# Kernel tuning notes

Measured on AMD Instinct MI355X. Metric: run time of the kernel, lower is better.

Reference implementation:

```python
import jax, jax.numpy as jnp
import numpy as np

N = 50000
E = 600000
D = 128
EPS = 1e-5  # nn.LayerNorm default eps


def gcn_conv(x, W, b, src, dst):
    # PyG GCNConv with add_self_loops=True, edge_weight=None (all ones),
    # symmetric normalization D^-1/2 (A+I) D^-1/2.
    h = x @ W                                        # [N, D]
    deg = jnp.zeros((N,), h.dtype).at[dst].add(1.0) + 1.0  # +1 for self loop
    dinv = jax.lax.rsqrt(deg)                        # deg >= 1, safe
    norm = dinv[src] * dinv[dst]                     # [E]
    msg = h[src] * norm[:, None]                     # [E, D] gather
    agg = jax.ops.segment_sum(msg, dst, num_segments=N)
    agg = agg + h * (dinv * dinv)[:, None]           # self-loop term
    return agg + b


def layer_norm(x, g, b):
    mu = jnp.mean(x, axis=-1, keepdims=True)
    var = jnp.mean(jnp.square(x - mu), axis=-1, keepdims=True)
    return (x - mu) * jax.lax.rsqrt(var + EPS) * g + b


def setup_inputs() -> dict:
    key = jax.random.key(0)
    ks = jax.random.split(key, 6)
    x = jax.random.normal(ks[0], (N, D), dtype=jnp.float32)
    edge_index = jax.random.randint(ks[1], (2, E), 0, N, dtype=jnp.int64)
    s = 1.0 / np.sqrt(D)
    W1 = jax.random.uniform(ks[2], (D, D), jnp.float32, -s, s)
    W2 = jax.random.uniform(ks[3], (D, D), jnp.float32, -s, s)
    b1 = jnp.zeros((D,), jnp.float32)
    b2 = jnp.zeros((D,), jnp.float32)
    ln1_g = jnp.ones((D,), jnp.float32)
    ln1_b = jnp.zeros((D,), jnp.float32)
    ln2_g = jnp.ones((D,), jnp.float32)
    ln2_b = jnp.zeros((D,), jnp.float32)
    return {"x": x, "edge_index": edge_index, "W1": W1, "b1": b1,
            "ln1_g": ln1_g, "ln1_b": ln1_b, "W2": W2, "b2": b2,
            "ln2_g": ln2_g, "ln2_b": ln2_b}


def reference(x, edge_index, W1, b1, ln1_g, ln1_b, W2, b2, ln2_g, ln2_b):
    src, dst = edge_index[0], edge_index[1]
    out = gcn_conv(x, W1, b1, src, dst)
    out = jax.nn.relu(layer_norm(out, ln1_g, ln1_b))  # dropout = identity (eval)
    out = gcn_conv(out, W2, b2, src, dst)
    out = jax.nn.relu(layer_norm(out, ln2_g, ln2_b))
    return out + x
```

## Files before the change

### kernel.cpp

```cpp
#include <hip/hip_runtime.h>
#include <hip/hip_fp16.h>

#define D 128
#define EPS 1e-5f
#define KB 64
#define NBSH 7
#define BUCKW 128

typedef unsigned int u32;
typedef unsigned short u16;
typedef unsigned char u8;
typedef __attribute__((ext_vector_type(8))) _Float16 half8;
typedef __attribute__((ext_vector_type(4))) float f32x4;
typedef __attribute__((ext_vector_type(2))) float f32x2;

__device__ inline u16 f2h(float x) {
  _Float16 t = (_Float16)x;
  return __builtin_bit_cast(u16, t);
}
__device__ inline u8 f2fp8(float x) {
  return (u8)(__builtin_amdgcn_cvt_pk_fp8_f32(x, x, 0, false) & 0xff);
}

__global__ __launch_bounds__(256) void k_prep(const float* __restrict__ W1,
                                              const float* __restrict__ W2,
                                              u16* __restrict__ Wt1,
                                              u16* __restrict__ Wt2) {
  int i = blockIdx.x * 256 + threadIdx.x;
  if (i < 2 * D * D) {
    const float* W = (i < D * D) ? W1 : W2;
    u16* Wt = (i < D * D) ? Wt1 : Wt2;
    int ii = i & (D * D - 1);
    int k = ii >> 7, c = ii & 127;
    Wt[c * D + k] = f2h(W[ii]);
  }
}

template <bool F32IN>
__device__ __forceinline__ void gemm_body(const void* __restrict__ in_,
                                          const u16* __restrict__ Wt,
                                          u8* __restrict__ out, int nrows,
                                          int blk) {
  const int tid = threadIdx.x;
  const int lane = tid & 63, wv = tid >> 6;
  const int m = lane & 15, q = lane >> 4;
  const int r0 = blk * 64 + wv * 16;
  const int rowa = min(r0 + m, nrows - 1);

  f32x4 acc[8];
#pragma unroll
  for (int ct = 0; ct < 8; ct++) acc[ct] = (f32x4)(0.0f);

#pragma unroll
  for (int kk = 0; kk < 4; kk++) {
    const int kbase = kk * 32 + q * 8;
    half8 a;
    if (F32IN) {
      const float* in = (const float*)in_;
      float4 v0 = *(const float4*)(in + (size_t)rowa * D + kbase);
      float4 v1 = *(const float4*)(in + (size_t)rowa * D + kbase + 4);
      a[0] = (_Float16)v0.x; a[1] = (_Float16)v0.y;
      a[2] = (_Float16)v0.z; a[3] = (_Float16)v0.w;
      a[4] = (_Float16)v1.x; a[5] = (_Float16)v1.y;
      a[6] = (_Float16)v1.z; a[7] = (_Float16)v1.w;
    } else {
      const u16* in = (const u16*)in_;
      a = *(const half8*)(in + (size_t)rowa * D + kbase);
    }
#pragma unroll
    for (int ct = 0; ct < 8; ct++) {
      half8 b = *(const half8*)(Wt + (ct * 16 + m) * D + kbase);
      acc[ct] = __builtin_amdgcn_mfma_f32_16x16x32_f16(a, b, acc[ct], 0, 0, 0);
    }
  }

#pragma unroll
  for (int ct = 0; ct < 8; ct++) {
#pragma unroll
    for (int rg = 0; rg < 4; rg++) {
      int rr = r0 + q * 4 + rg;
      if (rr < nrows) out[(size_t)rr * D + ct * 16 + m] = f2fp8(acc[ct][rg]);
    }
  }
}

__global__ __launch_bounds__(256) void k_count_gemm1(
    const int* __restrict__ dst, int* __restrict__ cnt, int E, int NB, int EPB,
    const float* __restrict__ x, const u16* __restrict__ Wt1,
    u8* __restrict__ A, int nrows) {
  if (blockIdx.x < (u32)KB) {
    __shared__ int hist[512];
    const int k = blockIdx.x, tid = threadIdx.x;
    for (int i = tid; i < NB; i += 256) hist[i] = 0;
    __syncthreads();
    const int e0 = k * EPB, e1 = min(E, e0 + EPB);
    for (int base = e0 + tid; base < e1; base += 2048) {
      int dd[8];
#pragma unroll
      for (int i = 0; i < 8; i++) {
        int e = base + i * 256;
        dd[i] = (e < e1) ? dst[e] : -1;
      }
#pragma unroll
      for (int i = 0; i < 8; i++)
        if (dd[i] >= 0) atomicAdd(&hist[dd[i] >> NBSH], 1);
    }
    __syncthreads();
    for (int b = tid; b < NB; b += 256) cnt[b * KB + k] = hist[b];
  } else {
    gemm_body<true>(x, Wt1, A, nrows, blockIdx.x - KB);
  }
}

__global__ __launch_bounds__(1024) void k_scan(int* __restrict__ cnt, int M,
                                               int NB, int* __restrict__ bsv,
                                               int E) {
  __shared__ int wt[16];
  const int tid = threadIdx.x;
  const int lane = tid & 63, wid = tid >> 6;
  const int chunks = (M + 1023) >> 10;
  int running = 0;
  int i = tid;
  int v = (i < M) ? cnt[i] : 0;
  for (int c = 0; c < chunks; c++) {
    int inext = i + 1024;
    int vnext = (c + 1 < chunks && inext < M) ? cnt[inext] : 0;
    int incl = v;
#pragma unroll
    for (int o = 1; o < 64; o <<= 1) {
      int t = __shfl_up(incl, o, 64);
      if (lane >= o) incl += t;
    }
    if (lane == 63) wt[wid] = incl;
    __syncthreads();
    int woff = 0, total = 0;
#pragma unroll
    for (int j = 0; j < 16; j++) {
      int t = wt[j];
      if (j < wid) woff += t;
      total += t;
    }
    int excl = running + woff + incl - v;
    if (i < M) {
      cnt[i] = excl;
      if ((i & (KB - 1)) == 0) bsv[i / KB] = excl;
    }
    running += total;
    __syncthreads();
    i = inext;
    v = vnext;
  }
  if (tid == 0) bsv[NB] = E;
}

__global__ __launch_bounds__(256) void k_scatter(
    const int* __restrict__ src, const int* __restrict__ dst,
    const int* __restrict__ cnt, u32* __restrict__ tmp, int E, int NB,
    int EPB) {
  __shared__ int off[512];
  const int k = blockIdx.x, tid = threadIdx.x;
  for (int b = tid; b < NB; b += 256) off[b] = cnt[b * KB + k];
  __syncthreads();
  const int e0 = k * EPB, e1 = min(E, e0 + EPB);
  for (int base = e0 + tid; base < e1; base += 2048) {
    int dd[8], ss[8];
#pragma unroll
    for (int i = 0; i < 8; i++) {
      int e = base + i * 256;
      dd[i] = (e < e1) ? dst[e] : -1;
      ss[i] = (e < e1) ? src[e] : 0;
    }
#pragma unroll
    for (int i = 0; i < 8; i++) {
      if (dd[i] >= 0) {
        int p = atomicAdd(&off[dd[i] >> NBSH], 1);
        tmp[p] = (u32)ss[i] | ((u32)(dd[i] & (BUCKW - 1)) << 16);
      }
    }
  }
}

__global__ __launch_bounds__(256) void k_bucket(
    const u32* __restrict__ tmp, const int* __restrict__ bsv,
    int4* __restrict__ meta, float* __restrict__ dinv,
    u32* __restrict__ csr, int N) {
  __shared__ int hist[BUCKW];
  __shared__ int sc[BUCKW];
  __shared__ int cur[BUCKW];
  const int b = blockIdx.x, tid = threadIdx.x;
  const int s0 = bsv[b], s1 = bsv[b + 1];
  if (tid < BUCKW) hist[tid] = 0;
  __syncthreads();
  for (int base = s0 + tid; base < s1; base += 1024) {
    int tt[4];
#pragma unroll
    for (int i = 0; i < 4; i++) {
      int idx = base + i * 256;
      tt[i] = (idx < s1) ? (int)tmp[idx] : -1;
    }
#pragma unroll
    for (int i = 0; i < 4; i++)
      if (tt[i] >= 0) atomicAdd(&hist[(tt[i] >> 16) & (BUCKW - 1)], 1);
  }
  __syncthreads();
  if (tid < BUCKW) sc[tid] = hist[tid];
  __syncthreads();
#pragma unroll
  for (int o = 1; o < BUCKW; o <<= 1) {
    int t = 0;
    if (tid < BUCKW && tid >= o) t = sc[tid - o];
    __syncthreads();
    if (tid < BUCKW) sc[tid] += t;
    __syncthreads();
  }
  if (tid < BUCKW) {
    int dg = hist[tid];
    int excl = sc[tid] - dg;
    cur[tid] = excl;
    int d = (b << NBSH) + tid;
    if (d < N) {
      float dv = rsqrtf((float)dg + 1.0f);
      meta[d] = make_int4(s0 + excl, dg, __builtin_bit_cast(int, dv), 0);
      dinv[d] = dv;
    }
  }
  __syncthreads();
  for (int base = s0 + tid; base < s1; base += 1024) {
    int tt[4];
#pragma unroll
    for (int i = 0; i < 4; i++) {
      int idx = base + i * 256;
      tt[i] = (idx < s1) ? (int)tmp[idx] : -1;
    }
#pragma unroll
    for (int i = 0; i < 4; i++) {
      if (tt[i] >= 0) {
        int r = atomicAdd(&cur[(tt[i] >> 16) & (BUCKW - 1)], 1);
        csr[s0 + r] = (u32)tt[i] & 0xffffu;
      }
    }
  }
}

__global__ __launch_bounds__(256) void k_weights(
    const int4* __restrict__ meta, const float* __restrict__ dinv,
    u32* __restrict__ csr, int N) {
  int gid = blockIdx.x * 256 + threadIdx.x;
  int r = gid >> 2, j0 = gid & 3;
  if (r >= N) return;
  int4 mt = meta[r];
  float dv = __builtin_bit_cast(float, mt.z);
  for (int j = j0; j < mt.y; j += 4) {
    u32 s = csr[mt.x + j];
    float w = dinv[s] * dv;
    csr[mt.x + j] = s | ((u32)f2h(w) << 16);
  }
}

#define ACC_EDGE(vv, ww)                                                     \
  {                                                                          \
    f32x2 p_;                                                                \
    p_ = __builtin_amdgcn_cvt_pk_f32_fp8(vv.x, false);                       \
    acc[0] = fmaf(p_[0], ww, acc[0]); acc[1] = fmaf(p_[1], ww, acc[1]);      \
    p_ = __builtin_amdgcn_cvt_pk_f32_fp8(vv.x, true);                        \
    acc[2] = fmaf(p_[0], ww, acc[2]); acc[3] = fmaf(p_[1], ww, acc[3]);      \
    p_ = __builtin_amdgcn_cvt_pk_f32_fp8(vv.y, false);                       \
    acc[4] = fmaf(p_[0], ww, acc[4]); acc[5] = fmaf(p_[1], ww, acc[5]);      \
    p_ = __builtin_amdgcn_cvt_pk_f32_fp8(vv.y, true);                        \
    acc[6] = fmaf(p_[0], ww, acc[6]); acc[7] = fmaf(p_[1], ww, acc[7]);      \
  }

__device__ __forceinline__ void gather_ln_core(
    const uint2* __restrict__ hb, const int4* __restrict__ meta,
    const u32* __restrict__ csr, const float* __restrict__ b,
    const float* __restrict__ g, const float* __restrict__ bln,
    int row, int n, int sl, float out[8]) {
  const bool valid = row < n;
  const int rc = valid ? row : 0;
  int4 mt = meta[rc];
  int beg = mt.x;
  int cnt = valid ? mt.y : 0;
  float dv = __builtin_bit_cast(float, mt.z);
  float sn = dv * dv;

  float acc[8];
  {
    uint2 su = hb[(size_t)rc * 16 + sl];
    f32x2 p0 = __builtin_amdgcn_cvt_pk_f32_fp8(su.x, false);
    f32x2 p1 = __builtin_amdgcn_cvt_pk_f32_fp8(su.x, true);
    f32x2 p2 = __builtin_amdgcn_cvt_pk_f32_fp8(su.y, false);
    f32x2 p3 = __builtin_amdgcn_cvt_pk_f32_fp8(su.y, true);
    acc[0] = p0[0] * sn; acc[1] = p0[1] * sn;
    acc[2] = p1[0] * sn; acc[3] = p1[1] * sn;
    acc[4] = p2[0] * sn; acc[5] = p2[1] * sn;
    acc[6] = p3[0] * sn; acc[7] = p3[1] * sn;
  }

  int cm = max(cnt, __shfl_xor(cnt, 16, 64));
  cm = max(cm, __shfl_xor(cm, 32, 64));

  u32 epre = 0u;
  if (sl < cnt) epre = csr[beg + sl];

  for (int j0 = 0; j0 < cm; j0 += 16) {
    u32 ecur = epre;
    epre = 0u;
    {
      int nj = j0 + 16;
      if (nj < cm && sl < cnt - nj) epre = csr[beg + nj + sl];
    }
    int mm = min(cm - j0, 16);
    for (int j = 0; j < mm; j += 8) {
      u32 e0 = __shfl(ecur, j + 0, 16), e1 = __shfl(ecur, j + 1, 16);
      u32 e2 = __shfl(ecur, j + 2, 16), e3 = __shfl(ecur, j + 3, 16);
      u32 e4 = __shfl(ecur, j + 4, 16), e5 = __shfl(ecur, j + 5, 16);
      u32 e6 = __shfl(ecur, j + 6, 16), e7 = __shfl(ecur, j + 7, 16);
      uint2 v0 = hb[(size_t)(e0 & 0xffffu) * 16 + sl];
      uint2 v1 = hb[(size_t)(e1 & 0xffffu) * 16 + sl];
      uint2 v2 = hb[(size_t)(e2 & 0xffffu) * 16 + sl];
      uint2 v3 = hb[(size_t)(e3 & 0xffffu) * 16 + sl];
      uint2 v4 = hb[(size_t)(e4 & 0xffffu) * 16 + sl];
      uint2 v5 = hb[(size_t)(e5 & 0xffffu) * 16 + sl];
      uint2 v6 = hb[(size_t)(e6 & 0xffffu) * 16 + sl];
      uint2 v7 = hb[(size_t)(e7 & 0xffffu) * 16 + sl];
      float w0 = (float)__builtin_bit_cast(_Float16, (u16)(e0 >> 16));
      float w1 = (float)__builtin_bit_cast(_Float16, (u16)(e1 >> 16));
      float w2 = (float)__builtin_bit_cast(_Float16, (u16)(e2 >> 16));
      float w3 = (float)__builtin_bit_cast(_Float16, (u16)(e3 >> 16));
      float w4 = (float)__builtin_bit_cast(_Float16, (u16)(e4 >> 16));
      float w5 = (float)__builtin_bit_cast(_Float16, (u16)(e5 >> 16));
      float w6 = (float)__builtin_bit_cast(_Float16, (u16)(e6 >> 16));
      float w7 = (float)__builtin_bit_cast(_Float16, (u16)(e7 >> 16));
      ACC_EDGE(v0, w0);
      ACC_EDGE(v1, w1);
      ACC_EDGE(v2, w2);
      ACC_EDGE(v3, w3);
      ACC_EDGE(v4, w4);
      ACC_EDGE(v5, w5);
      ACC_EDGE(v6, w6);
      ACC_EDGE(v7, w7);
    }
  }

  int d0 = sl * 8;
  float4 bb0 = *(const float4*)(b + d0);
  float4 bb1 = *(const float4*)(b + d0 + 4);
  float a0 = acc[0] + bb0.x, a1 = acc[1] + bb0.y;
  float a2 = acc[2] + bb0.z, a3 = acc[3] + bb0.w;
  float a4 = acc[4] + bb1.x, a5 = acc[5] + bb1.y;
  float a6 = acc[6] + bb1.z, a7 = acc[7] + bb1.w;

  float sum = ((a0 + a1) + (a2 + a3)) + ((a4 + a5) + (a6 + a7));
#pragma unroll
  for (int o = 8; o >= 1; o >>= 1) sum += __shfl_xor(sum, o, 16);
  float mu = sum * (1.0f / 128.0f);
  float e0 = a0 - mu, e1 = a1 - mu, e2 = a2 - mu, e3 = a3 - mu;
  float e4 = a4 - mu, e5 = a5 - mu, e6 = a6 - mu, e7 = a7 - mu;
  float vs = ((e0 * e0 + e1 * e1) + (e2 * e2 + e3 * e3)) +
             ((e4 * e4 + e5 * e5) + (e6 * e6 + e7 * e7));
#pragma unroll
  for (int o = 8; o >= 1; o >>= 1) vs += __shfl_xor(vs, o, 16);
  float inv = rsqrtf(vs * (1.0f / 128.0f) + EPS);

  float4 gg0 = *(const float4*)(g + d0);
  float4 gg1 = *(const float4*)(g + d0 + 4);
  float4 bl0 = *(const float4*)(bln + d0);
  float4 bl1 = *(const float4*)(bln + d0 + 4);
  out[0] = fmaxf(e0 * inv * gg0.x + bl0.x, 0.0f);
  out[1] = fmaxf(e1 * inv * gg0.y + bl0.y, 0.0f);
  out[2] = fmaxf(e2 * inv * gg0.z + bl0.z, 0.0f);
  out[3] = fmaxf(e3 * inv * gg0.w + bl0.w, 0.0f);
  out[4] = fmaxf(e4 * inv * gg1.x + bl1.x, 0.0f);
  out[5] = fmaxf(e5 * inv * gg1.y + bl1.y, 0.0f);
  out[6] = fmaxf(e6 * inv * gg1.z + bl1.z, 0.0f);
  out[7] = fmaxf(e7 * inv * gg1.w + bl1.w, 0.0f);
}

__global__ __launch_bounds__(512) void k_mid(
    const uint2* __restrict__ hb, const int4* __restrict__ meta,
    const u32* __restrict__ csr,
    const float* __restrict__ b, const float* __restrict__ g,
    const float* __restrict__ bln,
    const u16* __restrict__ Wt2, u8* __restrict__ outB, int n) {
  __shared__ alignas(16) u16 sY[64 * 136];
  const int tid = threadIdx.x;
  const int sl = tid & 15;
  const int row0 = blockIdx.x * 64;

  for (int p = 0; p < 2; p++) {
    int lr = p * 32 + (tid >> 4);
    int row = row0 + lr;
    float o[8];
    gather_ln_core(hb, meta, csr, b, g, bln, row, n, sl, o);
    uint4 pk;
    pk.x = ((u32)f2h(o[1]) << 16) | (u32)f2h(o[0]);
    pk.y = ((u32)f2h(o[3]) << 16) | (u32)f2h(o[2]);
    pk.z = ((u32)f2h(o[5]) << 16) | (u32)f2h(o[4]);
    pk.w = ((u32)f2h(o[7]) << 16) | (u32)f2h(o[6]);
    *(uint4*)(sY + lr * 136 + sl * 8) = pk;
  }
  __syncthreads();

  const int lane = tid & 63, wv = tid >> 6;
  const int m = lane & 15, q = lane >> 4;
  const int rt = wv & 3;
  const int ch = wv >> 2;
  f32x4 acc[4];
#pragma unroll
  for (int c = 0; c < 4; c++) acc[c] = (f32x4)(0.0f);
  const u16* ap = sY + (rt * 16 + m) * 136 + q * 8;
#pragma unroll
  for (int kk = 0; kk < 4; kk++) {
    half8 a = *(const half8*)(ap + kk * 32);
#pragma unroll
    for (int c = 0; c < 4; c++) {
      int ct = ch * 4 + c;
      half8 bfr = *(const half8*)(Wt2 + (ct * 16 + m) * D + kk * 32 + q * 8);
      acc[c] = __builtin_amdgcn_mfma_f32_16x16x32_f16(a, bfr, acc[c], 0, 0, 0);
    }
  }
#pragma unroll
  for (int c = 0; c < 4; c++) {
    int ct = ch * 4 + c;
#pragma unroll
    for (int rg = 0; rg < 4; rg++) {
      int rr = row0 + rt * 16 + q * 4 + rg;
      if (rr < n) outB[(size_t)rr * D + ct * 16 + m] = f2fp8(acc[c][rg]);
    }
  }
}

__global__ __launch_bounds__(256) void k_gather2(
    const uint2* __restrict__ hb, const int4* __restrict__ meta,
    const u32* __restrict__ csr,
    const float* __restrict__ b, const float* __restrict__ g,
    const float* __restrict__ bln, const float* __restrict__ resid,
    float* __restrict__ outf, int n) {
  const int tid = threadIdx.x;
  const int sl = tid & 15;
  const int row = blockIdx.x * 16 + (tid >> 4);
  float o[8];
  gather_ln_core(hb, meta, csr, b, g, bln, row, n, sl, o);
  if (row >= n) return;
  size_t base = (size_t)row * D + sl * 8;
  float4 r0 = *(const float4*)(resid + base);
  float4 r1 = *(const float4*)(resid + base + 4);
  *(float4*)(outf + base) =
      make_float4(o[0] + r0.x, o[1] + r0.y, o[2] + r0.z, o[3] + r0.w);
  *(float4*)(outf + base + 4) =
      make_float4(o[4] + r1.x, o[5] + r1.y, o[6] + r1.z, o[7] + r1.w);
}

extern "C" void kernel_launch(void* const* d_in, const int* in_sizes, int n_in,
                              void* d_out, int out_size, void* d_ws, size_t ws_size,
                              hipStream_t stream) {
  const float* x    = (const float*)d_in[0];
  const int*   ei   = (const int*)d_in[1];
  const float* W1   = (const float*)d_in[2];
  const float* b1   = (const float*)d_in[3];
  const float* g1   = (const float*)d_in[4];
  const float* bl1  = (const float*)d_in[5];
  const float* W2   = (const float*)d_in[6];
  const float* b2   = (const float*)d_in[7];
  const float* g2   = (const float*)d_in[8];
  const float* bl2  = (const float*)d_in[9];

  const int N = in_sizes[0] / D;
  const int E = in_sizes[1] / 2;
  const int* src = ei;
  const int* dst = ei + E;

  const int NB  = (N + BUCKW - 1) / BUCKW;
  const int M   = NB * KB;
  const int EPB = (E + KB - 1) / KB;
  const int GB  = (N + 63) / 64;

  size_t off = 0;
  auto walloc = [&](size_t bytes) {
    void* p = (char*)d_ws + off;
    off = (off + bytes + 255) & ~(size_t)255;
    return p;
  };
  int*   cnt   = (int*)walloc((size_t)M * 4);
  int*   bsv   = (int*)walloc((size_t)(NB + 1) * 4);
  u32*   tmp   = (u32*)walloc((size_t)E * 4);
  u32*   csr   = (u32*)walloc((size_t)E * 4);
  int4*  meta  = (int4*)walloc((size_t)N * 16);
  float* dinv  = (float*)walloc((size_t)N * 4);
  u8*    A     = (u8*)walloc((size_t)N * D);
  u8*    B     = (u8*)walloc((size_t)N * D);
  u16*   Wt1   = (u16*)walloc((size_t)D * D * 2);
  u16*   Wt2   = (u16*)walloc((size_t)D * D * 2);
  float* O     = (float*)d_out;

  k_prep<<<(2 * D * D + 255) / 256, 256, 0, stream>>>(W1, W2, Wt1, Wt2);
  k_count_gemm1<<<KB + GB, 256, 0, stream>>>(dst, cnt, E, NB, EPB, x, Wt1, A, N);
  k_scan<<<1, 1024, 0, stream>>>(cnt, M, NB, bsv, E);
  k_scatter<<<KB, 256, 0, stream>>>(src, dst, cnt, tmp, E, NB, EPB);
  k_bucket<<<NB, 256, 0, stream>>>(tmp, bsv, meta, dinv, csr, N);
  k_weights<<<(N * 4 + 255) / 256, 256, 0, stream>>>(meta, dinv, csr, N);
  k_mid<<<GB, 512, 0, stream>>>((const uint2*)A, meta, csr, b1, g1, bl1,
                                Wt2, B, N);
  k_gather2<<<(N + 15) / 16, 256, 0, stream>>>((const uint2*)B, meta, csr,
                                               b2, g2, bl2, x, O, N);
}
```

Before: 214.4 us.

## Split fused gather+GEMM mid kernel into separate gather and GEMM kernels

Result: faster. 207.8 us (-3.1%).

```diff
diff --git a/kernel.cpp b/kernel.cpp
--- a/kernel.cpp
+++ b/kernel.cpp
@@ -257,8 +257,9 @@
   }
 }
 
-#define ACC_EDGE(vv, ww)                                                     \
+#define ACC_EDGE(vv, ee)                                                     \
   {                                                                          \
+    float ww = (float)__builtin_bit_cast(_Float16, (u16)((ee) >> 16));       \
     f32x2 p_;                                                                \
     p_ = __builtin_amdgcn_cvt_pk_f32_fp8(vv.x, false);                       \
     acc[0] = fmaf(p_[0], ww, acc[0]); acc[1] = fmaf(p_[1], ww, acc[1]);      \
@@ -323,22 +324,14 @@
       uint2 v5 = hb[(size_t)(e5 & 0xffffu) * 16 + sl];
       uint2 v6 = hb[(size_t)(e6 & 0xffffu) * 16 + sl];
       uint2 v7 = hb[(size_t)(e7 & 0xffffu) * 16 + sl];
-      float w0 = (float)__builtin_bit_cast(_Float16, (u16)(e0 >> 16));
-      float w1 = (float)__builtin_bit_cast(_Float16, (u16)(e1 >> 16));
-      float w2 = (float)__builtin_bit_cast(_Float16, (u16)(e2 >> 16));
-      float w3 = (float)__builtin_bit_cast(_Float16, (u16)(e3 >> 16));
-      float w4 = (float)__builtin_bit_cast(_Float16, (u16)(e4 >> 16));
-      float w5 = (float)__builtin_bit_cast(_Float16, (u16)(e5 >> 16));
-      float w6 = (float)__builtin_bit_cast(_Float16, (u16)(e6 >> 16));
-      float w7 = (float)__builtin_bit_cast(_Float16, (u16)(e7 >> 16));
-      ACC_EDGE(v0, w0);
-      ACC_EDGE(v1, w1);
-      ACC_EDGE(v2, w2);
-      ACC_EDGE(v3, w3);
-      ACC_EDGE(v4, w4);
-      ACC_EDGE(v5, w5);
-      ACC_EDGE(v6, w6);
-      ACC_EDGE(v7, w7);
+      ACC_EDGE(v0, e0);
+      ACC_EDGE(v1, e1);
+      ACC_EDGE(v2, e2);
+      ACC_EDGE(v3, e3);
+      ACC_EDGE(v4, e4);
+      ACC_EDGE(v5, e5);
+      ACC_EDGE(v6, e6);
+      ACC_EDGE(v7, e7);
     }
   }
 
@@ -376,61 +369,33 @@
   out[7] = fmaxf(e7 * inv * gg1.w + bl1.w, 0.0f);
 }
 
-__global__ __launch_bounds__(512) void k_mid(
+__global__ __launch_bounds__(256, 8) void k_gather1(
     const uint2* __restrict__ hb, const int4* __restrict__ meta,
     const u32* __restrict__ csr,
     const float* __restrict__ b, const float* __restrict__ g,
     const float* __restrict__ bln,
-    const u16* __restrict__ Wt2, u8* __restrict__ outB, int n) {
-  __shared__ alignas(16) u16 sY[64 * 136];
+    u16* __restrict__ y1, int n) {
   const int tid = threadIdx.x;
   const int sl = tid & 15;
-  const int row0 = blockIdx.x * 64;
-
-  for (int p = 0; p < 2; p++) {
-    int lr = p * 32 + (tid >> 4);
-    int row = row0 + lr;
-    float o[8];
-    gather_ln_core(hb, meta, csr, b, g, bln, row, n, sl, o);
-    uint4 pk;
-    pk.x = ((u32)f2h(o[1]) << 16) | (u32)f2h(o[0]);
-    pk.y = ((u32)f2h(o[3]) << 16) | (u32)f2h(o[2]);
-    pk.z = ((u32)f2h(o[5]) << 16) | (u32)f2h(o[4]);
-    pk.w = ((u32)f2h(o[7]) << 16) | (u32)f2h(o[6]);
-    *(uint4*)(sY + lr * 136 + sl * 8) = pk;
-  }
-  __syncthreads();
-
-  const int lane = tid & 63, wv = tid >> 6;
-  const int m = lane & 15, q = lane >> 4;
-  const int rt = wv & 3;
-  const int ch = wv >> 2;
-  f32x4 acc[4];
-#pragma unroll
-  for (int c = 0; c < 4; c++) acc[c] = (f32x4)(0.0f);
-  const u16* ap = sY + (rt * 16 + m) * 136 + q * 8;
-#pragma unroll
-  for (int kk = 0; kk < 4; kk++) {
-    half8 a = *(const half8*)(ap + kk * 32);
-#pragma unroll
-    for (int c = 0; c < 4; c++) {
-      int ct = ch * 4 + c;
-      half8 bfr = *(const half8*)(Wt2 + (ct * 16 + m) * D + kk * 32 + q * 8);
-      acc[c] = __builtin_amdgcn_mfma_f32_16x16x32_f16(a, bfr, acc[c], 0, 0, 0);
-    }
-  }
-#pragma unroll
-  for (int c = 0; c < 4; c++) {
-    int ct = ch * 4 + c;
-#pragma unroll
-    for (int rg = 0; rg < 4; rg++) {
-      int rr = row0 + rt * 16 + q * 4 + rg;
-      if (rr < n) outB[(size_t)rr * D + ct * 16 + m] = f2fp8(acc[c][rg]);
-    }
-  }
-}
-
-__global__ __launch_bounds__(256) void k_gather2(
+  const int row = blockIdx.x * 16 + (tid >> 4);
+  float o[8];
+  gather_ln_core(hb, meta, csr, b, g, bln, row, n, sl, o);
+  if (row >= n) return;
+  uint4 pk;
+  pk.x = ((u32)f2h(o[1]) << 16) | (u32)f2h(o[0]);
+  pk.y = ((u32)f2h(o[3]) << 16) | (u32)f2h(o[2]);
+  pk.z = ((u32)f2h(o[5]) << 16) | (u32)f2h(o[4]);
+  pk.w = ((u32)f2h(o[7]) << 16) | (u32)f2h(o[6]);
+  *(uint4*)(y1 + (size_t)row * D + sl * 8) = pk;
+}
+
+__global__ __launch_bounds__(256) void k_gemm2(const u16* __restrict__ y1,
+                                               const u16* __restrict__ Wt2,
+                                               u8* __restrict__ outB, int n) {
+  gemm_body<false>(y1, Wt2, outB, n, blockIdx.x);
+}
+
+__global__ __launch_bounds__(256, 8) void k_gather2(
     const uint2* __restrict__ hb, const int4* __restrict__ meta,
     const u32* __restrict__ csr,
     const float* __restrict__ b, const float* __restrict__ g,
@@ -474,6 +439,7 @@
   const int M   = NB * KB;
   const int EPB = (E + KB - 1) / KB;
   const int GB  = (N + 63) / 64;
+  const int RB  = (N + 15) / 16;
 
   size_t off = 0;
   auto walloc = [&](size_t bytes) {
@@ -491,6 +457,7 @@
   u8*    B     = (u8*)walloc((size_t)N * D);
   u16*   Wt1   = (u16*)walloc((size_t)D * D * 2);
   u16*   Wt2   = (u16*)walloc((size_t)D * D * 2);
+  u16*   y1    = (u16*)walloc((size_t)N * D * 2);
   float* O     = (float*)d_out;
 
   k_prep<<<(2 * D * D + 255) / 256, 256, 0, stream>>>(W1, W2, Wt1, Wt2);
@@ -499,8 +466,9 @@
   k_scatter<<<KB, 256, 0, stream>>>(src, dst, cnt, tmp, E, NB, EPB);
   k_bucket<<<NB, 256, 0, stream>>>(tmp, bsv, meta, dinv, csr, N);
   k_weights<<<(N * 4 + 255) / 256, 256, 0, stream>>>(meta, dinv, csr, N);
-  k_mid<<<GB, 512, 0, stream>>>((const uint2*)A, meta, csr, b1, g1, bl1,
-                                Wt2, B, N);
-  k_gather2<<<(N + 15) / 16, 256, 0, stream>>>((const uint2*)B, meta, csr,
-                                               b2, g2, bl2, x, O, N);
-}
+  k_gather1<<<RB, 256, 0, stream>>>((const uint2*)A, meta, csr, b1, g1, bl1,
+                                    y1, N);
+  k_gemm2<<<GB, 256, 0, stream>>>(y1, Wt2, B, N);
+  k_gather2<<<RB, 256, 0, stream>>>((const uint2*)B, meta, csr,
+                                    b2, g2, bl2, x, O, N);
+}
```
